# Optimization experiments

Measured on AMD Instinct MI355X. Metric: run time of the kernel, lower is better.

## Reference

```python
import jax, jax.numpy as jnp
import numpy as np

B, N, D_VIS, D_LBL = 64, 256, 2048, 512
H, F_OUT = 8, 256            # n_heads, gat_out_per_head_dim
D_IN = D_VIS + D_LBL         # 2560, GAT input dim
D_GAT = H * F_OUT            # 2048, concat-heads output dim
D_EMB = 512                  # final_embedding_dim
ALPHA = 0.2                  # LeakyReLU negative slope


def setup_inputs() -> dict:
    key = jax.random.key(0)
    ks = jax.random.split(key, 9)
    visual_features = jax.random.normal(ks[0], (B, D_VIS), jnp.float32)
    labels_features = jax.random.normal(ks[1], (N, D_LBL), jnp.float32)
    adj = (jax.random.uniform(ks[2], (N, N)) < 0.1).astype(jnp.float32)
    label_adj_matrix = jnp.maximum(adj, jnp.eye(N, dtype=jnp.float32))
    s = 1.0 / np.sqrt(D_IN)
    W_gat = jax.random.uniform(ks[3], (D_IN, H, F_OUT), jnp.float32, -s, s)
    a_src = jax.random.uniform(ks[4], (H, F_OUT), jnp.float32, -s, s)
    a_dst = jax.random.uniform(ks[5], (H, F_OUT), jnp.float32, -s, s)
    sg = 1.0 / np.sqrt(D_GAT)
    pool_q = jax.random.uniform(ks[6], (D_GAT,), jnp.float32, -sg, sg)
    fc_W = jax.random.uniform(ks[7], (D_GAT, D_EMB), jnp.float32, -sg, sg)
    fc_b = jax.random.uniform(ks[8], (D_EMB,), jnp.float32, -sg, sg)
    return {"visual_features": visual_features, "labels_features": labels_features,
            "label_adj_matrix": label_adj_matrix, "W_gat": W_gat, "a_src": a_src,
            "a_dst": a_dst, "pool_q": pool_q, "fc_W": fc_W, "fc_b": fc_b}


def reference(visual_features, labels_features, label_adj_matrix,
              W_gat, a_src, a_dst, pool_q, fc_W, fc_b):
    # Build per-sample contextualized label node features: (B, N, D_IN)
    x = jnp.concatenate(
        [jnp.broadcast_to(labels_features[None], (B, N, D_LBL)),
         jnp.broadcast_to(visual_features[:, None, :], (B, N, D_VIS))], axis=-1)
    # Multi-head GAT layer, batched over B (the torch code loops over B)
    Wh = jnp.einsum('bnd,dhf->bnhf', x, W_gat)            # (B, N, H, F)
    src = jnp.einsum('bnhf,hf->bhn', Wh, a_src)           # (B, H, N)
    dst = jnp.einsum('bnhf,hf->bhn', Wh, a_dst)           # (B, H, N)
    e = src[:, :, :, None] + dst[:, :, None, :]           # (B, H, N, N)
    e = jnp.where(e > 0, e, ALPHA * e)                    # LeakyReLU
    mask = (label_adj_matrix > 0)[None, None]             # (1, 1, N, N)
    scores = jnp.where(mask, e, jnp.float32(-9e15))
    attn = jax.nn.softmax(scores, axis=-1)                # (B, H, N, N)
    out = jnp.einsum('bhij,bjhf->bihf', attn, Wh)         # (B, N, H, F)
    out = jax.nn.elu(out.reshape(B, N, D_GAT))            # concat heads + ELU
    # attention pooling over label nodes
    pw = jax.nn.softmax(jnp.einsum('bnd,d->bn', out, pool_q), axis=-1)
    pooled = jnp.einsum('bn,bnd->bd', pw, out)            # (B, D_GAT)
    return pooled @ fc_W + fc_b                           # (B, D_EMB)
```

## Files before the change

### kernel.cpp

```cpp
#include <hip/hip_runtime.h>
#include <hip/hip_bf16.h>
#include <math.h>

#define BB 64
#define NN 256
#define D_VIS 2048
#define D_LBL 512
#define HH 8
#define FF 256
#define DG 2048
#define DE 512
#define ALPHA 0.2f
#define PSTRIDE 264

using bf16 = __hip_bfloat16;
using short8 = __attribute__((ext_vector_type(8))) short;
using f32x4  = __attribute__((ext_vector_type(4))) float;
__device__ __forceinline__ float b2f(bf16 x) { return __bfloat162float(x); }
__device__ __forceinline__ unsigned short f2bs(float x) {
    bf16 h = __float2bfloat16(x);
    unsigned short u;
    __builtin_memcpy(&u, &h, 2);
    return u;
}

__global__ void __launch_bounds__(256) k_wh(const float* __restrict__ labels,
                                            const float* __restrict__ visual,
                                            const float* __restrict__ Wg,
                                            unsigned short* __restrict__ WhLbT,
                                            float* __restrict__ WhVz,
                                            const float* __restrict__ aSrc,
                                            const float* __restrict__ aDst,
                                            float* __restrict__ srcLp,
                                            float* __restrict__ dstLp,
                                            float* __restrict__ srcVp,
                                            float* __restrict__ dstVp) {
    __shared__ unsigned short As[32][72];
    __shared__ unsigned short Bs[64][72];
    const int t = threadIdx.x;
    const int w = t >> 6;
    const int lane = t & 63;
    const int l15 = lane & 15, quad = lane >> 4;
    const int n0 = blockIdx.x * 64;
    const int p2 = blockIdx.x & 3;
    const int y = blockIdx.y;
    const bool isL = (y < 8);
    const int q = y - 8;
    const int m0  = isL ? y * 32 : (q & 1) * 32;
    const int z   = isL ? 0 : (q >> 1);
    const int kb0 = z * 512;
    const float* A = isL ? labels : visual;
    const int lda  = isL ? D_LBL : D_VIS;
    const float* Wb = Wg + (isL ? 0 : (size_t)D_LBL * DG);

    f32x4 acc[2];
    acc[0] = (f32x4){0.f, 0.f, 0.f, 0.f};
    acc[1] = (f32x4){0.f, 0.f, 0.f, 0.f};

    for (int kc = 0; kc < 8; ++kc) {
        const int kb = kb0 + kc * 64;
#pragma unroll
        for (int p = 0; p < 2; ++p) {
            const int idx = t + 256 * p;
            const int r = idx >> 4, q4 = idx & 15;
            const float4 v = *(const float4*)(A + (size_t)(m0 + r) * lda + kb + 4 * q4);
            unsigned short s4[4] = {f2bs(v.x), f2bs(v.y), f2bs(v.z), f2bs(v.w)};
            __builtin_memcpy(&As[r][4 * q4], s4, 8);
        }
#pragma unroll
        for (int p = 0; p < 4; ++p) {
            const int kk = (t >> 4) + 16 * p;
            const int c4 = (t & 15) * 4;
            const float4 v = *(const float4*)(Wb + (size_t)(kb + kk) * DG + n0 + c4);
            Bs[c4 + 0][kk] = f2bs(v.x);
            Bs[c4 + 1][kk] = f2bs(v.y);
            Bs[c4 + 2][kk] = f2bs(v.z);
            Bs[c4 + 3][kk] = f2bs(v.w);
        }
        __syncthreads();
#pragma unroll
        for (int ks = 0; ks < 2; ++ks) {
            const short8 bf = *(const short8*)&Bs[w * 16 + l15][ks * 32 + quad * 8];
#pragma unroll
            for (int mi = 0; mi < 2; ++mi) {
                const short8 af = *(const short8*)&As[mi * 16 + l15][ks * 32 + quad * 8];
                acc[mi] = __builtin_amdgcn_mfma_f32_16x16x32_bf16(af, bf, acc[mi], 0, 0, 0);
            }
        }
        __syncthreads();
    }
    const int col = n0 + w * 16 + l15;
    const int h = col >> 8;
    const float as = aSrc[col], ad = aDst[col];
    if (isL) {
#pragma unroll
        for (int mi = 0; mi < 2; ++mi) {
            unsigned short s4[4];
#pragma unroll
            for (int r = 0; r < 4; ++r) s4[r] = f2bs(acc[mi][r]);
            __builtin_memcpy(&WhLbT[(size_t)col * NN + m0 + mi * 16 + quad * 4], s4, 8);
        }
#pragma unroll
        for (int mi = 0; mi < 2; ++mi)
#pragma unroll
            for (int r = 0; r < 4; ++r) {
                float sv = acc[mi][r] * as;
                float dv = acc[mi][r] * ad;
#pragma unroll
                for (int off = 1; off < 16; off <<= 1) {
                    sv += __shfl_xor(sv, off);
                    dv += __shfl_xor(dv, off);
                }
                if (l15 == 0) {
                    const int row = m0 + mi * 16 + quad * 4 + r;
                    srcLp[(p2 * NN + row) * HH + h] = sv;
                    dstLp[(p2 * NN + row) * HH + h] = dv;
                }
            }
    } else {
        float* Wv = WhVz + (size_t)z * BB * DG;
#pragma unroll
        for (int mi = 0; mi < 2; ++mi)
#pragma unroll
            for (int r = 0; r < 4; ++r)
                Wv[(size_t)(m0 + mi * 16 + quad * 4 + r) * DG + col] = acc[mi][r];
        const int pv = p2 * 4 + z;
#pragma unroll
        for (int mi = 0; mi < 2; ++mi)
#pragma unroll
            for (int r = 0; r < 4; ++r) {
                float sv = acc[mi][r] * as;
                float dv = acc[mi][r] * ad;
#pragma unroll
                for (int off = 1; off < 16; off <<= 1) {
                    sv += __shfl_xor(sv, off);
                    dv += __shfl_xor(dv, off);
                }
                if (l15 == 0) {
                    const int row = m0 + mi * 16 + quad * 4 + r;
                    srcVp[(pv * BB + row) * HH + h] = sv;
                    dstVp[(pv * BB + row) * HH + h] = dv;
                }
            }
    }
}

__global__ void __launch_bounds__(512, 4) k_gat(const unsigned short* __restrict__ WhLbT,
                                                const float* __restrict__ WhVz,
                                                const float* __restrict__ srcLp,
                                                const float* __restrict__ dstLp,
                                                const float* __restrict__ srcVp,
                                                const float* __restrict__ dstVp,
                                                const float* __restrict__ adj,
                                                const float* __restrict__ pool_q,
                                                bf16* __restrict__ outb,
                                                float* __restrict__ ps_p) {
    const int bid = blockIdx.x;
    const int h = bid & 7;
    const int b = bid >> 3;
    const int t = threadIdx.x;
    const int w = t >> 6;
    const int lane = t & 63;
    const int l15 = lane & 15, quad = lane >> 4;

    __shared__ __align__(16) unsigned short Pl[64][PSTRIDE];
    __shared__ __align__(16) float dls2[2 * NN];
    __shared__ float slsA[NN], slsC[NN], slsTE[NN];
    __shared__ float inv[64];
    __shared__ __align__(16) float pd[64][68];

    if (t < NN) {
        float dl = 0.f, sl = 0.f;
#pragma unroll
        for (int p = 0; p < 4; ++p) {
            dl += dstLp[(p * NN + t) * HH + h];
            sl += srcLp[(p * NN + t) * HH + h];
        }
        dls2[2 * t]     = __expf(dl);
        dls2[2 * t + 1] = __expf(ALPHA * dl);
        float c = 0.f;
#pragma unroll
        for (int p = 0; p < 16; ++p)
            c += srcVp[(p * BB + b) * HH + h] + dstVp[(p * BB + b) * HH + h];
        const float u = c + sl;
        slsA[t]  = __expf(u);
        slsC[t]  = __expf(ALPHA * u);
        slsTE[t] = __expf(-u);
    }
    const int n0 = w * 32;
    float wv[2] = {0.f, 0.f};
#pragma unroll
    for (int z = 0; z < 4; ++z)
#pragma unroll
        for (int ni = 0; ni < 2; ++ni)
            wv[ni] += WhVz[(size_t)z * BB * DG + (size_t)b * DG + h * FF + n0 + ni * 16 + l15];
    const float pqv0 = pool_q[h * FF + n0 + l15];
    const float pqv1 = pool_q[h * FF + n0 + 16 + l15];
    const unsigned short* wb = WhLbT + (size_t)(h * FF + n0 + l15) * NN + quad * 8;
    __syncthreads();

    for (int it = 0; it < 4; ++it) {
        const int i0 = it * 64;

        {
            const int g = lane >> 4, s = lane & 15;
#pragma unroll
            for (int rr = 0; rr < 2; ++rr) {
                const int iloc = w * 8 + rr * 4 + g;
                const int i = i0 + iloc;
                const float Ai = slsA[i], Ci = slsC[i], TEi = slsTE[i];
                float pr[16];
                float sum = 0.f;
#pragma unroll
                for (int jj = 0; jj < 8; ++jj) {
                    const int j0 = 2 * s + 32 * jj;
                    const float2 av = *(const float2*)(adj + (size_t)i * NN + j0);
                    const float4 bd = *(const float4*)&dls2[2 * j0];
                    const bool g0 = bd.x > TEi;
                    const bool g1 = bd.z > TEi;
                    float p0 = (g0 ? Ai : Ci) * (g0 ? bd.x : bd.y);
                    float p1 = (g1 ? Ai : Ci) * (g1 ? bd.z : bd.w);
                    p0 = av.x > 0.f ? p0 : 0.f;
                    p1 = av.y > 0.f ? p1 : 0.f;
                    pr[2 * jj] = p0; pr[2 * jj + 1] = p1;
                    sum += p0 + p1;
                }
#pragma unroll
                for (int off = 1; off < 16; off <<= 1) sum += __shfl_xor(sum, off);
                if (s == 0) inv[iloc] = 1.0f / sum;
#pragma unroll
                for (int jj = 0; jj < 8; ++jj) {
                    const unsigned int pk =
                        ((unsigned int)f2bs(pr[2 * jj + 1]) << 16) | f2bs(pr[2 * jj]);
                    *(unsigned int*)&Pl[iloc][2 * s + 32 * jj] = pk;
                }
            }
        }
        __syncthreads();

        f32x4 acc[4][2];
#pragma unroll
        for (int mi = 0; mi < 4; ++mi)
#pragma unroll
            for (int ni = 0; ni < 2; ++ni) acc[mi][ni] = (f32x4){0.f, 0.f, 0.f, 0.f};

        short8 bc0 = *(const short8*)(wb);
        short8 bc1 = *(const short8*)(wb + (size_t)16 * NN);
#pragma unroll
        for (int kc = 0; kc < 8; ++kc) {
            short8 bn0, bn1;
            if (kc < 7) {
                bn0 = *(const short8*)(wb + (kc + 1) * 32);
                bn1 = *(const short8*)(wb + (size_t)16 * NN + (kc + 1) * 32);
            }
            short8 a[4];
#pragma unroll
            for (int mi = 0; mi < 4; ++mi)
                a[mi] = *(const short8*)&Pl[mi * 16 + l15][kc * 32 + quad * 8];
#pragma unroll
            for (int mi = 0; mi < 4; ++mi)
                acc[mi][0] = __builtin_amdgcn_mfma_f32_16x16x32_bf16(a[mi], bc0, acc[mi][0], 0, 0, 0);
#pragma unroll
            for (int mi = 0; mi < 4; ++mi)
                acc[mi][1] = __builtin_amdgcn_mfma_f32_16x16x32_bf16(a[mi], bc1, acc[mi][1], 0, 0, 0);
            bc0 = bn0; bc1 = bn1;
        }

#pragma unroll
        for (int mi = 0; mi < 4; ++mi)
#pragma unroll
            for (int r = 0; r < 4; ++r) {
                const int row = mi * 16 + quad * 4 + r;
                const float ivr = inv[row];
                bf16* orow = outb + ((size_t)(b * NN + i0 + row)) * DG + h * FF + n0;
                float x0 = fmaf(acc[mi][0][r], ivr, wv[0]);
                float x1 = fmaf(acc[mi][1][r], ivr, wv[1]);
                x0 = x0 > 0.f ? x0 : (__expf(x0) - 1.0f);
                x1 = x1 > 0.f ? x1 : (__expf(x1) - 1.0f);
                orow[l15]      = __float2bfloat16(x0);
                orow[16 + l15] = __float2bfloat16(x1);
                float dot = fmaf(x0, pqv0, x1 * pqv1);
                dot += __shfl_xor(dot, 8);
                if (l15 < 8) pd[row][w * 8 + l15] = dot;
            }
        __syncthreads();
        if (t < 64) {
            float s4 = 0.f;
#pragma unroll
            for (int i = 0; i < 16; ++i) {
                const f32x4 v = *(const f32x4*)&pd[t][4 * i];
                s4 += v[0] + v[1] + v[2] + v[3];
            }
            ps_p[((size_t)h * BB + b) * NN + i0 + t] = s4;
        }
    }
}

__global__ void __launch_bounds__(256) k_pool(const bf16* __restrict__ outb,
                                              const float* __restrict__ ps_p,
                                              float* __restrict__ pooled,
                                              const float* __restrict__ fcb,
                                              float* __restrict__ out) {
    const int dt = blockIdx.x;
    const int b  = blockIdx.y;
    const int t  = threadIdx.x;
    if (dt < 2) out[b * DE + dt * 256 + t] = fcb[dt * 256 + t];
    __shared__ float wsm[NN];
    __shared__ float redm[4];
    __shared__ float reds[4];
    float v = 0.f;
#pragma unroll
    for (int s = 0; s < 8; ++s)
        v += ps_p[((size_t)s * BB + b) * NN + t];
    float m = v;
#pragma unroll
    for (int off = 32; off; off >>= 1) m = fmaxf(m, __shfl_xor(m, off));
    if ((t & 63) == 0) redm[t >> 6] = m;
    __syncthreads();
    m = fmaxf(fmaxf(redm[0], redm[1]), fmaxf(redm[2], redm[3]));
    const float e = __expf(v - m);
    float s = e;
#pragma unroll
    for (int off = 32; off; off >>= 1) s += __shfl_xor(s, off);
    if ((t & 63) == 0) reds[t >> 6] = s;
    __syncthreads();
    s = reds[0] + reds[1] + reds[2] + reds[3];
    wsm[t] = e / s;
    __syncthreads();
    const int d = dt * 256 + t;
    float acc = 0.f;
    const bf16* base = outb + (size_t)b * NN * DG + d;
#pragma unroll 8
    for (int n = 0; n < NN; ++n)
        acc = fmaf(wsm[n], b2f(base[(size_t)n * DG]), acc);
    pooled[(size_t)b * DG + d] = acc;
}

__global__ void __launch_bounds__(256) k_mgemm(const float* __restrict__ A, int lda,
                                               const float* __restrict__ W, int ldw,
                                               float* __restrict__ C, int ldc,
                                               int kSlice, int kIters) {
    __shared__ unsigned short As[32][72];
    __shared__ unsigned short Bs[64][72];
    const int t = threadIdx.x;
    const int w = t >> 6;
    const int lane = t & 63;
    const int l15 = lane & 15, quad = lane >> 4;
    const int n0 = blockIdx.x * 64;
    const int m0 = blockIdx.y * 32;
    const int kb0 = blockIdx.z * kSlice;
    f32x4 acc[2];
    acc[0] = (f32x4){0.f, 0.f, 0.f, 0.f};
    acc[1] = (f32x4){0.f, 0.f, 0.f, 0.f};
    for (int kc = 0; kc < kIters; ++kc) {
        const int kb = kb0 + kc * 64;
#pragma unroll
        for (int p = 0; p < 2; ++p) {
            const int idx = t + 256 * p;
            const int r = idx >> 4, q4 = idx & 15;
            const float4 v = *(const float4*)(A + (size_t)(m0 + r) * lda + kb + 4 * q4);
            unsigned short s4[4] = {f2bs(v.x), f2bs(v.y), f2bs(v.z), f2bs(v.w)};
            __builtin_memcpy(&As[r][4 * q4], s4, 8);
        }
#pragma unroll
        for (int p = 0; p < 4; ++p) {
            const int kk = (t >> 4) + 16 * p;
            const int c4 = (t & 15) * 4;
            const float4 v = *(const float4*)(W + (size_t)(kb + kk) * ldw + n0 + c4);
            Bs[c4 + 0][kk] = f2bs(v.x);
            Bs[c4 + 1][kk] = f2bs(v.y);
            Bs[c4 + 2][kk] = f2bs(v.z);
            Bs[c4 + 3][kk] = f2bs(v.w);
        }
        __syncthreads();
#pragma unroll
        for (int ks = 0; ks < 2; ++ks) {
            const short8 bf = *(const short8*)&Bs[w * 16 + l15][ks * 32 + quad * 8];
#pragma unroll
            for (int mi = 0; mi < 2; ++mi) {
                const short8 af = *(const short8*)&As[mi * 16 + l15][ks * 32 + quad * 8];
                acc[mi] = __builtin_amdgcn_mfma_f32_16x16x32_bf16(af, bf, acc[mi], 0, 0, 0);
            }
        }
        __syncthreads();
    }
    const int col = n0 + w * 16 + l15;
#pragma unroll
    for (int mi = 0; mi < 2; ++mi)
#pragma unroll
        for (int r = 0; r < 4; ++r)
            atomicAdd(&C[(size_t)(m0 + mi * 16 + quad * 4 + r) * ldc + col], acc[mi][r]);
}

extern "C" void kernel_launch(void* const* d_in, const int* in_sizes, int n_in,
                              void* d_out, int out_size, void* d_ws, size_t ws_size,
                              hipStream_t stream) {
    (void)in_sizes; (void)n_in; (void)out_size; (void)ws_size;
    const float* visual = (const float*)d_in[0];
    const float* labels = (const float*)d_in[1];
    const float* adj    = (const float*)d_in[2];
    const float* Wg     = (const float*)d_in[3];
    const float* a_src  = (const float*)d_in[4];
    const float* a_dst  = (const float*)d_in[5];
    const float* pool_q = (const float*)d_in[6];
    const float* fcW    = (const float*)d_in[7];
    const float* fcb    = (const float*)d_in[8];
    float* out = (float*)d_out;

    float* ws_f   = (float*)d_ws;
    float* WhVz   = ws_f;
    float* srcLp  = WhVz + 4 * BB * DG;
    float* dstLp  = srcLp + 4 * NN * HH;
    float* srcVp  = dstLp + 4 * NN * HH;
    float* dstVp  = srcVp + 16 * BB * HH;
    float* ps_p   = dstVp + 16 * BB * HH;
    float* pooled = ps_p + 8 * BB * NN;
    bf16*  outb   = (bf16*)(pooled + BB * DG);
    unsigned short* WhLbT = (unsigned short*)(outb + (size_t)BB * NN * DG);

    k_wh<<<dim3(DG / 64, 16), 256, 0, stream>>>(labels, visual, Wg, WhLbT, WhVz,
                                                a_src, a_dst, srcLp, dstLp, srcVp, dstVp);

    k_gat<<<BB * HH, 512, 0, stream>>>(WhLbT, WhVz, srcLp, dstLp, srcVp, dstVp,
                                       adj, pool_q, outb, ps_p);

    k_pool<<<dim3(8, BB), 256, 0, stream>>>(outb, ps_p, pooled, fcb, out);

    k_mgemm<<<dim3(DE / 64, BB / 32, 8), 256, 0, stream>>>(
        pooled, DG, fcW, DE, out, DE, 256, 4);
}
```

Before: 190.0 us.

## Pack adjacency into bitmask, enlarge k_wh M-tile, simplify pool-dot reduction

Extra blocks in the Wh projection kernel turn the float adjacency matrix into a 16-bit-per-lane bitmask, so k_gat reads packed bits instead of float2 adjacency values for every head and batch. The k_wh M-tile grows from 32 to 64 rows, halving the grid and reusing each B tile across more MFMAs. The pooling-score reduction now uses a full 16-lane shuffle into a small [8][64] shared array instead of the padded [64][68] buffer. The cost is less parallelism in k_wh and more shuffles per row in k_gat.

```diff
diff --git a/kernel.cpp b/kernel.cpp
--- a/kernel.cpp
+++ b/kernel.cpp
@@ -34,33 +34,50 @@
                                             float* __restrict__ srcLp,
                                             float* __restrict__ dstLp,
                                             float* __restrict__ srcVp,
-                                            float* __restrict__ dstVp) {
-    __shared__ unsigned short As[32][72];
+                                            float* __restrict__ dstVp,
+                                            const float* __restrict__ adj,
+                                            unsigned short* __restrict__ abits) {
+    const int t = threadIdx.x;
+    const int y = blockIdx.y;
+    if (y == 8) {
+        if (t < 128) {
+            const int r = t >> 4, s = t & 15;
+            const int i = blockIdx.x * 8 + r;
+            unsigned int bits = 0;
+#pragma unroll
+            for (int jj = 0; jj < 8; ++jj) {
+                const float2 av = *(const float2*)(adj + (size_t)i * NN + 2 * s + 32 * jj);
+                bits |= (av.x > 0.f ? 1u : 0u) << (2 * jj);
+                bits |= (av.y > 0.f ? 1u : 0u) << (2 * jj + 1);
+            }
+            abits[i * 16 + s] = (unsigned short)bits;
+        }
+        return;
+    }
+
+    __shared__ unsigned short As[64][72];
     __shared__ unsigned short Bs[64][72];
-    const int t = threadIdx.x;
     const int w = t >> 6;
     const int lane = t & 63;
     const int l15 = lane & 15, quad = lane >> 4;
     const int n0 = blockIdx.x * 64;
     const int p2 = blockIdx.x & 3;
-    const int y = blockIdx.y;
-    const bool isL = (y < 8);
-    const int q = y - 8;
-    const int m0  = isL ? y * 32 : (q & 1) * 32;
-    const int z   = isL ? 0 : (q >> 1);
+    const bool isL = (y < 4);
+    const int m0  = isL ? y * 64 : 0;
+    const int z   = isL ? 0 : (y - 4);
     const int kb0 = z * 512;
     const float* A = isL ? labels : visual;
     const int lda  = isL ? D_LBL : D_VIS;
     const float* Wb = Wg + (isL ? 0 : (size_t)D_LBL * DG);
 
-    f32x4 acc[2];
-    acc[0] = (f32x4){0.f, 0.f, 0.f, 0.f};
-    acc[1] = (f32x4){0.f, 0.f, 0.f, 0.f};
+    f32x4 acc[4];
+#pragma unroll
+    for (int mi = 0; mi < 4; ++mi) acc[mi] = (f32x4){0.f, 0.f, 0.f, 0.f};
 
     for (int kc = 0; kc < 8; ++kc) {
         const int kb = kb0 + kc * 64;
 #pragma unroll
-        for (int p = 0; p < 2; ++p) {
+        for (int p = 0; p < 4; ++p) {
             const int idx = t + 256 * p;
             const int r = idx >> 4, q4 = idx & 15;
             const float4 v = *(const float4*)(A + (size_t)(m0 + r) * lda + kb + 4 * q4);
@@ -82,7 +99,7 @@
         for (int ks = 0; ks < 2; ++ks) {
             const short8 bf = *(const short8*)&Bs[w * 16 + l15][ks * 32 + quad * 8];
 #pragma unroll
-            for (int mi = 0; mi < 2; ++mi) {
+            for (int mi = 0; mi < 4; ++mi) {
                 const short8 af = *(const short8*)&As[mi * 16 + l15][ks * 32 + quad * 8];
                 acc[mi] = __builtin_amdgcn_mfma_f32_16x16x32_bf16(af, bf, acc[mi], 0, 0, 0);
             }
@@ -94,14 +111,14 @@
     const float as = aSrc[col], ad = aDst[col];
     if (isL) {
 #pragma unroll
-        for (int mi = 0; mi < 2; ++mi) {
+        for (int mi = 0; mi < 4; ++mi) {
             unsigned short s4[4];
 #pragma unroll
             for (int r = 0; r < 4; ++r) s4[r] = f2bs(acc[mi][r]);
             __builtin_memcpy(&WhLbT[(size_t)col * NN + m0 + mi * 16 + quad * 4], s4, 8);
         }
 #pragma unroll
-        for (int mi = 0; mi < 2; ++mi)
+        for (int mi = 0; mi < 4; ++mi)
 #pragma unroll
             for (int r = 0; r < 4; ++r) {
                 float sv = acc[mi][r] * as;
@@ -120,13 +137,13 @@
     } else {
         float* Wv = WhVz + (size_t)z * BB * DG;
 #pragma unroll
-        for (int mi = 0; mi < 2; ++mi)
+        for (int mi = 0; mi < 4; ++mi)
 #pragma unroll
             for (int r = 0; r < 4; ++r)
-                Wv[(size_t)(m0 + mi * 16 + quad * 4 + r) * DG + col] = acc[mi][r];
+                Wv[(size_t)(mi * 16 + quad * 4 + r) * DG + col] = acc[mi][r];
         const int pv = p2 * 4 + z;
 #pragma unroll
-        for (int mi = 0; mi < 2; ++mi)
+        for (int mi = 0; mi < 4; ++mi)
 #pragma unroll
             for (int r = 0; r < 4; ++r) {
                 float sv = acc[mi][r] * as;
@@ -137,7 +154,7 @@
                     dv += __shfl_xor(dv, off);
                 }
                 if (l15 == 0) {
-                    const int row = m0 + mi * 16 + quad * 4 + r;
+                    const int row = mi * 16 + quad * 4 + r;
                     srcVp[(pv * BB + row) * HH + h] = sv;
                     dstVp[(pv * BB + row) * HH + h] = dv;
                 }
@@ -151,7 +168,7 @@
                                                 const float* __restrict__ dstLp,
                                                 const float* __restrict__ srcVp,
                                                 const float* __restrict__ dstVp,
-                                                const float* __restrict__ adj,
+                                                const unsigned short* __restrict__ abits,
                                                 const float* __restrict__ pool_q,
                                                 bf16* __restrict__ outb,
                                                 float* __restrict__ ps_p) {
@@ -167,7 +184,7 @@
     __shared__ __align__(16) float dls2[2 * NN];
     __shared__ float slsA[NN], slsC[NN], slsTE[NN];
     __shared__ float inv[64];
-    __shared__ __align__(16) float pd[64][68];
+    __shared__ float psl[8][64];
 
     if (t < NN) {
         float dl = 0.f, sl = 0.f;
@@ -208,20 +225,20 @@
             for (int rr = 0; rr < 2; ++rr) {
                 const int iloc = w * 8 + rr * 4 + g;
                 const int i = i0 + iloc;
+                const unsigned int mb = abits[i * 16 + s];
                 const float Ai = slsA[i], Ci = slsC[i], TEi = slsTE[i];
                 float pr[16];
                 float sum = 0.f;
 #pragma unroll
                 for (int jj = 0; jj < 8; ++jj) {
                     const int j0 = 2 * s + 32 * jj;
-                    const float2 av = *(const float2*)(adj + (size_t)i * NN + j0);
                     const float4 bd = *(const float4*)&dls2[2 * j0];
                     const bool g0 = bd.x > TEi;
                     const bool g1 = bd.z > TEi;
                     float p0 = (g0 ? Ai : Ci) * (g0 ? bd.x : bd.y);
                     float p1 = (g1 ? Ai : Ci) * (g1 ? bd.z : bd.w);
-                    p0 = av.x > 0.f ? p0 : 0.f;
-                    p1 = av.y > 0.f ? p1 : 0.f;
+                    p0 = (mb & (1u << (2 * jj)))     ? p0 : 0.f;
+                    p1 = (mb & (1u << (2 * jj + 1))) ? p1 : 0.f;
                     pr[2 * jj] = p0; pr[2 * jj + 1] = p1;
                     sum += p0 + p1;
                 }
@@ -280,18 +297,16 @@
                 orow[l15]      = __float2bfloat16(x0);
                 orow[16 + l15] = __float2bfloat16(x1);
                 float dot = fmaf(x0, pqv0, x1 * pqv1);
-                dot += __shfl_xor(dot, 8);
-                if (l15 < 8) pd[row][w * 8 + l15] = dot;
+#pragma unroll
+                for (int off = 1; off < 16; off <<= 1) dot += __shfl_xor(dot, off);
+                if (l15 == 0) psl[w][row] = dot;
             }
         __syncthreads();
         if (t < 64) {
-            float s4 = 0.f;
-#pragma unroll
-            for (int i = 0; i < 16; ++i) {
-                const f32x4 v = *(const f32x4*)&pd[t][4 * i];
-                s4 += v[0] + v[1] + v[2] + v[3];
-            }
-            ps_p[((size_t)h * BB + b) * NN + i0 + t] = s4;
+            float s = 0.f;
+#pragma unroll
+            for (int ww = 0; ww < 8; ++ww) s += psl[ww][t];
+            ps_p[((size_t)h * BB + b) * NN + i0 + t] = s;
         }
     }
 }
@@ -417,12 +432,14 @@
     float* pooled = ps_p + 8 * BB * NN;
     bf16*  outb   = (bf16*)(pooled + BB * DG);
     unsigned short* WhLbT = (unsigned short*)(outb + (size_t)BB * NN * DG);
-
-    k_wh<<<dim3(DG / 64, 16), 256, 0, stream>>>(labels, visual, Wg, WhLbT, WhVz,
-                                                a_src, a_dst, srcLp, dstLp, srcVp, dstVp);
+    unsigned short* abits = WhLbT + (size_t)DG * NN;
+
+    k_wh<<<dim3(DG / 64, 9), 256, 0, stream>>>(labels, visual, Wg, WhLbT, WhVz,
+                                               a_src, a_dst, srcLp, dstLp, srcVp, dstVp,
+                                               adj, abits);
 
     k_gat<<<BB * HH, 512, 0, stream>>>(WhLbT, WhVz, srcLp, dstLp, srcVp, dstVp,
-                                       adj, pool_q, outb, ps_p);
+                                       abits, pool_q, outb, ps_p);
 
     k_pool<<<dim3(8, BB), 256, 0, stream>>>(outb, ps_p, pooled, fcb, out);
 
```

New measurement: 178.6 us. 1.06x faster.
